# Optimization experiments

Hardware: AMD Instinct MI355X
Metric: run time of the kernel (lower is better)

The kernel has to match this reference:

```python
import jax, jax.numpy as jnp
import numpy as np

WINDOW = (2, 7, 7)
SHIFT = (1, 3, 3)
HEADS = 4


def _rel_pos_index(ws):
    coords = np.stack(np.meshgrid(*[np.arange(w) for w in ws], indexing='ij'))  # (3, wd, wh, ww)
    cf = coords.reshape(3, -1)
    rel = cf[:, :, None] - cf[:, None, :]  # (3, N, N)
    rel = rel.transpose(1, 2, 0).astype(np.int64)
    rel[:, :, 0] += ws[0] - 1
    rel[:, :, 1] += ws[1] - 1
    rel[:, :, 2] += ws[2] - 1
    rel[:, :, 0] *= (2 * ws[1] - 1) * (2 * ws[2] - 1)
    rel[:, :, 1] *= 2 * ws[2] - 1
    return rel.sum(-1)  # (N, N)


def _attn_mask(D, H, W, ws, ss):
    img = np.zeros((1, D, H, W, 1), np.float32)
    cnt = 0
    for d in (slice(None, -ws[0]), slice(-ws[0], -ss[0]), slice(-ss[0], None)):
        for h in (slice(None, -ws[1]), slice(-ws[1], -ss[1]), slice(-ss[1], None)):
            for w in (slice(None, -ws[2]), slice(-ws[2], -ss[2]), slice(-ss[2], None)):
                img[:, d, h, w, :] = cnt
                cnt += 1
    N = ws[0] * ws[1] * ws[2]
    mw = img.reshape(1, D // ws[0], ws[0], H // ws[1], ws[1], W // ws[2], ws[2], 1)
    mw = mw.transpose(0, 1, 3, 5, 2, 4, 6, 7).reshape(-1, N)  # (nW, N)
    diff = mw[:, None, :] - mw[:, :, None]
    return np.where(diff != 0, -100.0, 0.0).astype(np.float32)  # (nW, N, N)


def _win_partition(x, ws):
    B, D, H, W, C = x.shape
    x = x.reshape(B, D // ws[0], ws[0], H // ws[1], ws[1], W // ws[2], ws[2], C)
    return x.transpose(0, 1, 3, 5, 2, 4, 6, 7).reshape(-1, ws[0] * ws[1] * ws[2], C)


def _win_reverse(win, ws, B, D, H, W):
    C = win.shape[-1]
    x = win.reshape(B, D // ws[0], H // ws[1], W // ws[2], ws[0], ws[1], ws[2], C)
    return x.transpose(0, 1, 4, 2, 5, 3, 6, 7).reshape(B, D, H, W, C)


def _ln(x, w, b):
    mu = x.mean(-1, keepdims=True)
    var = x.var(-1, keepdims=True)
    return (x - mu) / jnp.sqrt(var + 1e-5) * w + b


def setup_inputs() -> dict:
    key = jax.random.key(0)
    ks = jax.random.split(key, 8)
    B, D, H, W, C = 4, 8, 56, 56, 128
    hidden = 4 * C
    table = (2 * WINDOW[0] - 1) * (2 * WINDOW[1] - 1) * (2 * WINDOW[2] - 1)
    return {
        'x': jax.random.normal(ks[0], (B, D, H, W, C), jnp.float32),
        'norm1_w': jnp.ones((C,), jnp.float32),
        'norm1_b': jnp.zeros((C,), jnp.float32),
        'qkv_w': 0.02 * jax.random.normal(ks[1], (3 * C, C), jnp.float32),
        'qkv_b': jnp.zeros((3 * C,), jnp.float32),
        'rpb': 0.02 * jax.random.normal(ks[2], (table, HEADS), jnp.float32),
        'proj_w': 0.02 * jax.random.normal(ks[3], (C, C), jnp.float32),
        'proj_b': jnp.zeros((C,), jnp.float32),
        'norm2_w': jnp.ones((C,), jnp.float32),
        'norm2_b': jnp.zeros((C,), jnp.float32),
        'fc1_w': 0.02 * jax.random.normal(ks[4], (hidden, C), jnp.float32),
        'fc1_b': jnp.zeros((hidden,), jnp.float32),
        'fc2_w': 0.02 * jax.random.normal(ks[5], (C, hidden), jnp.float32),
        'fc2_b': jnp.zeros((C,), jnp.float32),
    }


def reference(x, norm1_w, norm1_b, qkv_w, qkv_b, rpb, proj_w, proj_b,
              norm2_w, norm2_b, fc1_w, fc1_b, fc2_w, fc2_b):
    B, D, H, W, C = x.shape
    hd = C // HEADS
    scale = hd ** -0.5
    N = WINDOW[0] * WINDOW[1] * WINDOW[2]

    shortcut = x
    y = _ln(x, norm1_w, norm1_b)
    # cyclic shift (SW-MSA)
    y = jnp.roll(y, (-SHIFT[0], -SHIFT[1], -SHIFT[2]), axis=(1, 2, 3))
    win = _win_partition(y, WINDOW)  # (B_, N, C)
    B_ = win.shape[0]

    qkv = win @ qkv_w.T + qkv_b  # (B_, N, 3C)
    qkv = qkv.reshape(B_, N, 3, HEADS, hd).transpose(2, 0, 3, 1, 4)
    q, k, v = qkv[0] * scale, qkv[1], qkv[2]  # (B_, h, N, hd)

    attn = jnp.einsum('bhnd,bhmd->bhnm', q, k)  # (B_, h, N, N)
    rpi = _rel_pos_index(WINDOW)
    bias = rpb[rpi.reshape(-1)].reshape(N, N, HEADS).transpose(2, 0, 1)  # (h, N, N)
    attn = attn + bias[None]

    mask = jnp.asarray(_attn_mask(D, H, W, WINDOW, SHIFT))  # (nW, N, N)
    nW = mask.shape[0]
    attn = attn.reshape(B_ // nW, nW, HEADS, N, N) + mask[None, :, None]
    attn = jax.nn.softmax(attn.reshape(B_, HEADS, N, N), axis=-1)

    out = jnp.einsum('bhnm,bhmd->bhnd', attn, v)
    out = out.transpose(0, 2, 1, 3).reshape(B_, N, C)
    out = out @ proj_w.T + proj_b

    y = _win_reverse(out, WINDOW, B, D, H, W)
    y = jnp.roll(y, SHIFT, axis=(1, 2, 3))  # reverse cyclic shift
    x = shortcut + y

    h = _ln(x, norm2_w, norm2_b)
    h = jax.nn.gelu(h @ fc1_w.T + fc1_b, approximate=False)
    h = h @ fc2_w.T + fc2_b
    return x + h
```

## Files before the change

### kernel.cpp

```cpp
#include <hip/hip_runtime.h>
#include <math.h>

typedef short bf16x8 __attribute__((ext_vector_type(8)));
typedef float f32x4 __attribute__((ext_vector_type(4)));
typedef unsigned short u16;

#define DEVFN static __device__ __forceinline__

DEVFN u16 f2bf(float f) {
  union { float f; unsigned u; } v; v.f = f;
  return (u16)((v.u + 0x7FFFu + ((v.u >> 16) & 1u)) >> 16);
}

DEVFN void gload16(const void* g, void* l) {
  __builtin_amdgcn_global_load_lds(
      (const __attribute__((address_space(1))) void*)g,
      (__attribute__((address_space(3))) void*)l, 16, 0, 0);
}

DEVFN float gelu_tanh(float x) {
  float x2 = x * x;
  float m = x * fmaf(0.044715f, x2, 1.0f);
  float e = __expf(-1.5957691216057308f * m);
  return x / (1.0f + e);
}

#define TT 100352
#define BWIN 1024

__global__ void convert4_kernel(const float* __restrict__ a, const float* __restrict__ b,
                                const float* __restrict__ c, const float* __restrict__ d,
                                u16* __restrict__ oa, u16* __restrict__ ob,
                                u16* __restrict__ oc, u16* __restrict__ od) {
  int i = blockIdx.x * 256 + threadIdx.x;
  const float* s; u16* o; int off;
  if (i < 49152)       { s = a; o = oa; off = i; }
  else if (i < 65536)  { s = b; o = ob; off = i - 49152; }
  else if (i < 131072) { s = c; o = oc; off = i - 65536; }
  else                 { s = d; o = od; off = i - 131072; }
  o[off] = f2bf(s[off]);
}

__global__ void bias_kernel(const float* __restrict__ rpb, float* __restrict__ bias_full) {
  int idx = blockIdx.x * 256 + threadIdx.x;
  if (idx >= 4 * 9604) return;
  int h = idx / 9604, rem = idx % 9604, i = rem / 98, j = rem % 98;
  int di = i / 49, ri = i % 49, hi = ri / 7, wi = ri % 7;
  int dj = j / 49, rj = j % 49, hj = rj / 7, wj = rj % 7;
  int tidx = (di - dj + 1) * 169 + (hi - hj + 6) * 13 + (wi - wj + 6);
  bias_full[idx] = rpb[tidx * 4 + h];
}

template<int SHIFTED>
__global__ __launch_bounds__(256) void ln_kernel(const float* __restrict__ x,
    const float* __restrict__ w, const float* __restrict__ bterm, u16* __restrict__ out)
{
  int gw = blockIdx.x * 4 + (threadIdx.x >> 6);
  int lane = threadIdx.x & 63;
  size_t src;
  if (SHIFTED) {
    int b_ = gw / 98, n = gw % 98;
    int bb = b_ >> 8, widx = b_ & 255;
    int dw = widx >> 6, hw = (widx >> 3) & 7, ww = widx & 7;
    int dd = n / 49, rr = n % 49, hh = rr / 7, wn = rr % 7;
    int d = (dw * 2 + dd + 1) & 7;
    int h = hw * 7 + hh + 3; if (h >= 56) h -= 56;
    int wq = ww * 7 + wn + 3; if (wq >= 56) wq -= 56;
    src = ((size_t)(((bb * 8 + d) * 56 + h) * 56 + wq)) * 128;
  } else {
    src = (size_t)gw * 128;
  }
  float2 v = *(const float2*)(x + src + lane * 2);
  float s = v.x + v.y, q = v.x * v.x + v.y * v.y;
  #pragma unroll
  for (int m = 1; m < 64; m <<= 1) { s += __shfl_xor(s, m, 64); q += __shfl_xor(q, m, 64); }
  float mu = s * (1.0f / 128.0f);
  float var = q * (1.0f / 128.0f) - mu * mu;
  float rstd = rsqrtf(var + 1e-5f);
  int c = lane * 2;
  float y0 = (v.x - mu) * rstd * w[c] + bterm[c];
  float y1 = (v.y - mu) * rstd * w[c + 1] + bterm[c + 1];
  ushort2 o; o.x = f2bf(y0); o.y = f2bf(y1);
  *(ushort2*)(out + (size_t)gw * 128 + c) = o;
}

template<int EPI>
__global__ __launch_bounds__(256) void gemm_kernel(
    const u16* __restrict__ A, const u16* __restrict__ Bw,
    const float* __restrict__ bias, const float* __restrict__ res,
    void* __restrict__ outp, int M, int N, int K)
{
  __shared__ u16 smem[16384];
  u16* As = smem;
  u16* Bs = smem + 8192;
  const int m0 = blockIdx.x * 128, n0 = blockIdx.y * 128;
  const int t = threadIdx.x;
  const int wid = t >> 6, lane = t & 63;
  const int wr = wid >> 1, wc = wid & 1;
  const int l15 = lane & 15, lhi = lane >> 4;
  const int srow = lane >> 3;
  const int sslot = lane & 7;
  const int gcol = ((sslot ^ srow) << 3);
  f32x4 acc[4][4] = {};
  for (int k0 = 0; k0 < K; k0 += 64) {
    #pragma unroll
    for (int it = 0; it < 4; ++it) {
      const int rbase = it * 32 + wid * 8;
      const int row = rbase + srow;
      gload16(A + (size_t)(m0 + row) * K + k0 + gcol, As + rbase * 64);
      gload16(Bw + (size_t)(n0 + row) * K + k0 + gcol, Bs + rbase * 64);
    }
    __syncthreads();
    #pragma unroll
    for (int kk = 0; kk < 64; kk += 32) {
      bf16x8 af[4], bfr[4];
      const int csw = (kk + lhi * 8) ^ ((l15 & 7) << 3);
      #pragma unroll
      for (int mi = 0; mi < 4; ++mi) af[mi] = *(const bf16x8*)(As + (wr * 64 + mi * 16 + l15) * 64 + csw);
      #pragma unroll
      for (int ni = 0; ni < 4; ++ni) bfr[ni] = *(const bf16x8*)(Bs + (wc * 64 + ni * 16 + l15) * 64 + csw);
      #pragma unroll
      for (int mi = 0; mi < 4; ++mi)
        #pragma unroll
        for (int ni = 0; ni < 4; ++ni)
          acc[mi][ni] = __builtin_amdgcn_mfma_f32_16x16x32_bf16(af[mi], bfr[ni], acc[mi][ni], 0, 0, 0);
    }
    __syncthreads();
  }
  if (EPI == 0) {
    const float smul = (n0 == 0) ? 0.17677669529663689f : 1.0f;
    #pragma unroll
    for (int mi = 0; mi < 4; ++mi)
      #pragma unroll
      for (int ni = 0; ni < 4; ++ni) {
        int col = wc * 64 + ni * 16 + l15;
        float bcol = bias[n0 + col];
        #pragma unroll
        for (int r = 0; r < 4; ++r) {
          int row = wr * 64 + mi * 16 + lhi * 4 + r;
          float v = (acc[mi][ni][r] + bcol) * smul;
          smem[row * 128 + (((col >> 3) ^ (row & 7)) << 3) + (col & 7)] = f2bf(v);
        }
      }
    __syncthreads();
    const int rsub = t >> 4, sl = t & 15;
    #pragma unroll
    for (int j = 0; j < 8; ++j) {
      int row = j * 16 + rsub;
      int4 val = *(const int4*)(smem + row * 128 + ((sl ^ (row & 7)) << 3));
      *(int4*)((u16*)outp + (size_t)(m0 + row) * N + n0 + sl * 8) = val;
    }
  } else {
    #pragma unroll
    for (int mi = 0; mi < 4; ++mi)
      #pragma unroll
      for (int r = 0; r < 4; ++r) {
        int row = m0 + wr * 64 + mi * 16 + lhi * 4 + r;
        int b_ = row / 98, n = row % 98;
        int bb = b_ >> 8, widx = b_ & 255;
        int dw = widx >> 6, hw = (widx >> 3) & 7, ww = widx & 7;
        int dd = n / 49, rr = n % 49, hh = rr / 7, wn = rr % 7;
        int d = (dw * 2 + dd + 1) & 7;
        int h = hw * 7 + hh + 3; if (h >= 56) h -= 56;
        int wq = ww * 7 + wn + 3; if (wq >= 56) wq -= 56;
        size_t dbase = ((size_t)(((bb * 8 + d) * 56 + h) * 56 + wq)) * 128;
        #pragma unroll
        for (int ni = 0; ni < 4; ++ni) {
          int col = n0 + wc * 64 + ni * 16 + l15;
          float v = acc[mi][ni][r] + bias[col];
          ((float*)outp)[dbase + col] = res[dbase + col] + v;
        }
      }
  }
}

__global__ __launch_bounds__(256) void mlp_kernel(
    const u16* __restrict__ A, const u16* __restrict__ W1, const float* __restrict__ b1,
    const u16* __restrict__ W2, const float* __restrict__ b2,
    const float* __restrict__ res, float* __restrict__ outp)
{
  __shared__ u16 smem[32768];
  u16* As = smem;
  u16* Ws = smem + 8192;
  u16* Hs = smem + 24576;
  const int m0 = blockIdx.x * 64;
  const int t = threadIdx.x, wid = t >> 6, lane = t & 63;
  const int wr = wid >> 1, wc = wid & 1;
  const int l15 = lane & 15, lhi = lane >> 4;
  const int lrow4 = lane >> 4;
  const int lslot = lane & 15;

  #pragma unroll
  for (int i = 0; i < 4; ++i) {
    int row = i * 16 + wid * 4 + lrow4;
    gload16(A + (size_t)(m0 + row) * 128 + ((lslot ^ (row & 7)) << 3), As + i * 2048 + wid * 512);
  }
  #pragma unroll
  for (int i = 0; i < 8; ++i) {
    int row = i * 16 + wid * 4 + lrow4;
    gload16(W1 + (size_t)row * 128 + ((lslot ^ (row & 7)) << 3), Ws + i * 2048 + wid * 512);
  }
  f32x4 accO[2][4] = {};
  for (int hc = 0; hc < 4; ++hc) {
    __syncthreads();
    f32x4 accH[2][4] = {};
    #pragma unroll
    for (int kk = 0; kk < 128; kk += 32) {
      bf16x8 af[2], bfr[4];
      #pragma unroll
      for (int mi = 0; mi < 2; ++mi) {
        int row = wr * 32 + mi * 16 + l15;
        af[mi] = *(const bf16x8*)(As + row * 128 + (((((kk >> 3) + lhi)) ^ (row & 7)) << 3));
      }
      #pragma unroll
      for (int ni = 0; ni < 4; ++ni) {
        int row = wc * 64 + ni * 16 + l15;
        bfr[ni] = *(const bf16x8*)(Ws + row * 128 + (((((kk >> 3) + lhi)) ^ (row & 7)) << 3));
      }
      #pragma unroll
      for (int mi = 0; mi < 2; ++mi)
        #pragma unroll
        for (int ni = 0; ni < 4; ++ni)
          accH[mi][ni] = __builtin_amdgcn_mfma_f32_16x16x32_bf16(af[mi], bfr[ni], accH[mi][ni], 0, 0, 0);
    }
    __syncthreads();
    #pragma unroll
    for (int i = 0; i < 8; ++i) {
      int row = i * 16 + wid * 4 + lrow4;
      gload16(W2 + (size_t)row * 512 + hc * 128 + ((lslot ^ (row & 7)) << 3), Ws + i * 2048 + wid * 512);
    }
    #pragma unroll
    for (int mi = 0; mi < 2; ++mi)
      #pragma unroll
      for (int ni = 0; ni < 4; ++ni) {
        int hid = wc * 64 + ni * 16 + l15;
        float bb = b1[hc * 128 + hid];
        #pragma unroll
        for (int r = 0; r < 4; ++r) {
          int tok = wr * 32 + mi * 16 + lhi * 4 + r;
          float g = gelu_tanh(accH[mi][ni][r] + bb);
          Hs[tok * 128 + (((hid >> 3) ^ (tok & 7)) << 3) + (hid & 7)] = f2bf(g);
        }
      }
    __syncthreads();
    #pragma unroll
    for (int kk = 0; kk < 128; kk += 32) {
      bf16x8 af[2], bfr[4];
      #pragma unroll
      for (int mi = 0; mi < 2; ++mi) {
        int row = wr * 32 + mi * 16 + l15;
        af[mi] = *(const bf16x8*)(Hs + row * 128 + (((((kk >> 3) + lhi)) ^ (row & 7)) << 3));
      }
      #pragma unroll
      for (int ni = 0; ni < 4; ++ni) {
        int row = wc * 64 + ni * 16 + l15;
        bfr[ni] = *(const bf16x8*)(Ws + row * 128 + (((((kk >> 3) + lhi)) ^ (row & 7)) << 3));
      }
      #pragma unroll
      for (int mi = 0; mi < 2; ++mi)
        #pragma unroll
        for (int ni = 0; ni < 4; ++ni)
          accO[mi][ni] = __builtin_amdgcn_mfma_f32_16x16x32_bf16(af[mi], bfr[ni], accO[mi][ni], 0, 0, 0);
    }
    if (hc < 3) {
      __syncthreads();
      #pragma unroll
      for (int i = 0; i < 8; ++i) {
        int row = i * 16 + wid * 4 + lrow4;
        gload16(W1 + (size_t)((hc + 1) * 128 + row) * 128 + ((lslot ^ (row & 7)) << 3),
                Ws + i * 2048 + wid * 512);
      }
    }
  }
  #pragma unroll
  for (int mi = 0; mi < 2; ++mi)
    #pragma unroll
    for (int r = 0; r < 4; ++r) {
      int tok = m0 + wr * 32 + mi * 16 + lhi * 4 + r;
      #pragma unroll
      for (int ni = 0; ni < 4; ++ni) {
        int col = wc * 64 + ni * 16 + l15;
        size_t dst = (size_t)tok * 128 + col;
        outp[dst] = accO[mi][ni][r] + b2[col] + res[dst];
      }
    }
}

__global__ __launch_bounds__(64) void attn_kernel(
    const u16* __restrict__ qkv, const float* __restrict__ bias_full,
    u16* __restrict__ out_win)
{
  __shared__ u16 vT[32][136];
  __shared__ u16 P[16][136];
  __shared__ signed char rids[112];
  const int bid = blockIdx.x;
  const int w = bid >> 2, h = bid & 3;
  const int lane = threadIdx.x;
  const int l15 = lane & 15, lhi = lane >> 4;
  const int widx = w & 255;
  const int dw = widx >> 6, hw = (widx >> 3) & 7, ww = widx & 7;

  #pragma unroll
  for (int rep = 0; rep < 2; ++rep) {
    int t2 = lane + rep * 64;
    if (t2 < 112) {
      int rv = 0;
      if (t2 < 98) {
        int dd = t2 / 49, rr = t2 % 49, hh = rr / 7, wn = rr % 7;
        int dp = dw * 2 + dd, hp = hw * 7 + hh, wp = ww * 7 + wn;
        int rd = dp < 6 ? 0 : (dp < 7 ? 1 : 2);
        int rh = hp < 49 ? 0 : (hp < 53 ? 1 : 2);
        int rw2 = wp < 49 ? 0 : (wp < 53 ? 1 : 2);
        rv = rd * 9 + rh * 3 + rw2;
      }
      rids[t2] = (signed char)rv;
    }
  }
  for (int f = lane; f < 160; f += 64) {
    int d = f / 5, c = 96 + (f % 5) * 8;
    *(int4*)&vT[d][c] = (int4){0, 0, 0, 0};
  }
  if (lane < 48) {
    int r = lane / 3, c = 112 + (lane % 3) * 8;
    *(int4*)&P[r][c] = (int4){0, 0, 0, 0};
  }
  const size_t base = (size_t)w * 98 * 384;
  for (int f = lane; f < 392; f += 64) {
    int n = f >> 2, c = (f & 3) * 8;
    int4 v = *(const int4*)(qkv + base + (size_t)n * 384 + 256 + h * 32 + c);
    const u16* pv = (const u16*)&v;
    #pragma unroll
    for (int j = 0; j < 8; ++j) vT[c + j][n] = pv[j];
  }
  __syncthreads();

  const float* bh = bias_full + h * 9604;
  const size_t obase = (size_t)w * 98 * 128;
  for (int mt = 0; mt < 7; ++mt) {
    int qn = mt * 16 + l15; if (qn > 97) qn = 97;
    bf16x8 aq = *(const bf16x8*)(qkv + base + (size_t)qn * 384 + h * 32 + lhi * 8);
    f32x4 sf[7];
    #pragma unroll
    for (int nt = 0; nt < 7; ++nt) {
      int kn = nt * 16 + l15; if (kn > 97) kn = 97;
      bf16x8 bk = *(const bf16x8*)(qkv + base + (size_t)kn * 384 + 128 + h * 32 + lhi * 8);
      f32x4 z = {0.f, 0.f, 0.f, 0.f};
      sf[nt] = __builtin_amdgcn_mfma_f32_16x16x32_bf16(aq, bk, z, 0, 0, 0);
    }
    int irow[4], ridr[4];
    #pragma unroll
    for (int r = 0; r < 4; ++r) {
      irow[r] = mt * 16 + lhi * 4 + r;
      ridr[r] = rids[irow[r] > 111 ? 111 : irow[r]];
    }
    float mx[4] = {-1e30f, -1e30f, -1e30f, -1e30f};
    #pragma unroll
    for (int nt = 0; nt < 7; ++nt) {
      int j = nt * 16 + l15;
      int jc = j > 97 ? 97 : j;
      int rj = rids[j];
      #pragma unroll
      for (int r = 0; r < 4; ++r) {
        float s = sf[nt][r];
        int ic = irow[r] > 97 ? 97 : irow[r];
        s += bh[ic * 98 + jc];
        if (ridr[r] != rj) s -= 100.0f;
        if (j > 97) s = -1e30f;
        sf[nt][r] = s;
        mx[r] = fmaxf(mx[r], s);
      }
    }
    #pragma unroll
    for (int m = 1; m < 16; m <<= 1)
      #pragma unroll
      for (int r = 0; r < 4; ++r) mx[r] = fmaxf(mx[r], __shfl_xor(mx[r], m, 64));
    float sm[4] = {0.f, 0.f, 0.f, 0.f};
    #pragma unroll
    for (int nt = 0; nt < 7; ++nt)
      #pragma unroll
      for (int r = 0; r < 4; ++r) {
        float p = __expf(sf[nt][r] - mx[r]);
        sf[nt][r] = p;
        sm[r] += p;
      }
    #pragma unroll
    for (int m = 1; m < 16; m <<= 1)
      #pragma unroll
      for (int r = 0; r < 4; ++r) sm[r] += __shfl_xor(sm[r], m, 64);
    float inv[4];
    #pragma unroll
    for (int r = 0; r < 4; ++r) inv[r] = 1.0f / sm[r];
    __syncthreads();
    #pragma unroll
    for (int nt = 0; nt < 7; ++nt)
      #pragma unroll
      for (int r = 0; r < 4; ++r)
        P[lhi * 4 + r][nt * 16 + l15] = f2bf(sf[nt][r] * inv[r]);
    __syncthreads();
    f32x4 o0 = {}, o1 = {};
    #pragma unroll
    for (int ks = 0; ks < 4; ++ks) {
      bf16x8 ap  = *(const bf16x8*)(&P[l15][ks * 32 + lhi * 8]);
      bf16x8 bv0 = *(const bf16x8*)(&vT[l15][ks * 32 + lhi * 8]);
      bf16x8 bv1 = *(const bf16x8*)(&vT[16 + l15][ks * 32 + lhi * 8]);
      o0 = __builtin_amdgcn_mfma_f32_16x16x32_bf16(ap, bv0, o0, 0, 0, 0);
      o1 = __builtin_amdgcn_mfma_f32_16x16x32_bf16(ap, bv1, o1, 0, 0, 0);
    }
    #pragma unroll
    for (int r = 0; r < 4; ++r) {
      if (irow[r] < 98) {
        size_t orow = obase + (size_t)irow[r] * 128 + h * 32;
        out_win[orow + l15] = f2bf(o0[r]);
        out_win[orow + 16 + l15] = f2bf(o1[r]);
      }
    }
  }
}

extern "C" void kernel_launch(void* const* d_in, const int* in_sizes, int n_in,
                              void* d_out, int out_size, void* d_ws, size_t ws_size,
                              hipStream_t stream)
{
  const float* x      = (const float*)d_in[0];
  const float* n1w    = (const float*)d_in[1];
  const float* n1b    = (const float*)d_in[2];
  const float* qkv_w  = (const float*)d_in[3];
  const float* qkv_b  = (const float*)d_in[4];
  const float* rpb    = (const float*)d_in[5];
  const float* proj_w = (const float*)d_in[6];
  const float* proj_b = (const float*)d_in[7];
  const float* n2w    = (const float*)d_in[8];
  const float* n2b    = (const float*)d_in[9];
  const float* fc1_w  = (const float*)d_in[10];
  const float* fc1_b  = (const float*)d_in[11];
  const float* fc2_w  = (const float*)d_in[12];
  const float* fc2_b  = (const float*)d_in[13];

  char* p = (char*)d_ws;
  size_t off = 0;
  auto alloc = [&](size_t bytes) { void* r = p + off; off = (off + bytes + 255) & ~(size_t)255; return r; };
  u16*   qkvw_b    = (u16*)alloc(49152 * 2);
  u16*   projw_b   = (u16*)alloc(16384 * 2);
  u16*   fc1w_b    = (u16*)alloc(65536 * 2);
  u16*   fc2w_b    = (u16*)alloc(65536 * 2);
  float* bias_full = (float*)alloc(4 * 9604 * 4);
  u16*   y_win     = (u16*)alloc((size_t)TT * 128 * 2);
  float* x2        = (float*)alloc((size_t)TT * 128 * 4);
  u16*   h1        = (u16*)alloc((size_t)TT * 128 * 2);
  u16*   big       = (u16*)alloc((size_t)TT * 384 * 2);
  if (off > ws_size) return;

  convert4_kernel<<<768, 256, 0, stream>>>(qkv_w, proj_w, fc1_w, fc2_w,
                                           qkvw_b, projw_b, fc1w_b, fc2w_b);
  bias_kernel<<<(4 * 9604 + 255) / 256, 256, 0, stream>>>(rpb, bias_full);
  ln_kernel<1><<<TT / 4, 256, 0, stream>>>(x, n1w, n1b, y_win);
  gemm_kernel<0><<<dim3(TT / 128, 3), 256, 0, stream>>>(y_win, qkvw_b, qkv_b, nullptr, big, TT, 384, 128);
  attn_kernel<<<BWIN * 4, 64, 0, stream>>>(big, bias_full, y_win);
  gemm_kernel<1><<<dim3(TT / 128, 1), 256, 0, stream>>>(y_win, projw_b, proj_b, x, x2, TT, 128, 128);
  ln_kernel<0><<<TT / 4, 256, 0, stream>>>(x2, n2w, n2b, h1);
  mlp_kernel<<<TT / 64, 256, 0, stream>>>(h1, fc1w_b, fc1_b, fc2w_b, fc2_b, x2, (float*)d_out);
}
```

Baseline: 235.0 us.

## Restructure MLP kernel with 64-wide hidden chunks, register A, smaller LDS

The fused MLP kernel now processes the 512-wide hidden dimension in eight 64-wide chunks instead of four 128-wide chunks. It keeps the activation tile in registers rather than LDS and uses separate W1 and W2 chunk buffers, with W2 prefetched during the first GEMM. LDS drops from 64KB to 40KB and launch bounds request 4 blocks per CU, aiming for higher occupancy and better latency hiding. The cost is more barriers and chunk loads per block, and extra register pressure from holding A in registers.

```diff
diff --git a/kernel.cpp b/kernel.cpp
--- a/kernel.cpp
+++ b/kernel.cpp
@@ -174,101 +174,105 @@
   }
 }
 
-__global__ __launch_bounds__(256) void mlp_kernel(
+__global__ __launch_bounds__(256, 4) void mlp_kernel(
     const u16* __restrict__ A, const u16* __restrict__ W1, const float* __restrict__ b1,
     const u16* __restrict__ W2, const float* __restrict__ b2,
     const float* __restrict__ res, float* __restrict__ outp)
 {
-  __shared__ u16 smem[32768];
-  u16* As = smem;
-  u16* Ws = smem + 8192;
-  u16* Hs = smem + 24576;
+  __shared__ u16 smem[20480];
+  u16* W1c = smem;
+  u16* W2c = smem + 8192;
+  u16* Hs  = smem + 16384;
   const int m0 = blockIdx.x * 64;
   const int t = threadIdx.x, wid = t >> 6, lane = t & 63;
   const int wr = wid >> 1, wc = wid & 1;
   const int l15 = lane & 15, lhi = lane >> 4;
-  const int lrow4 = lane >> 4;
-  const int lslot = lane & 15;
+  const int srow4 = lane >> 4, sslot16 = lane & 15;
+  const int srow8 = lane >> 3, sslot8 = lane & 7;
 
   #pragma unroll
-  for (int i = 0; i < 4; ++i) {
-    int row = i * 16 + wid * 4 + lrow4;
-    gload16(A + (size_t)(m0 + row) * 128 + ((lslot ^ (row & 7)) << 3), As + i * 2048 + wid * 512);
-  }
+  for (int it = 0; it < 4; ++it) {
+    int rb1 = it * 16 + wid * 4;
+    gload16(W1 + (size_t)(rb1 + srow4) * 128 + ((sslot16 ^ ((rb1 + srow4) & 7)) << 3),
+            W1c + rb1 * 128);
+    int rb2 = it * 32 + wid * 8;
+    gload16(W2 + (size_t)(rb2 + srow8) * 512 + ((sslot8 ^ ((rb2 + srow8) & 7)) << 3),
+            W2c + rb2 * 64);
+  }
+  bf16x8 areg[2][4];
   #pragma unroll
-  for (int i = 0; i < 8; ++i) {
-    int row = i * 16 + wid * 4 + lrow4;
-    gload16(W1 + (size_t)row * 128 + ((lslot ^ (row & 7)) << 3), Ws + i * 2048 + wid * 512);
-  }
+  for (int mi = 0; mi < 2; ++mi)
+    #pragma unroll
+    for (int kg = 0; kg < 4; ++kg)
+      areg[mi][kg] = *(const bf16x8*)(A + (size_t)(m0 + wr * 32 + mi * 16 + l15) * 128 + kg * 32 + lhi * 8);
+
   f32x4 accO[2][4] = {};
-  for (int hc = 0; hc < 4; ++hc) {
-    __syncthreads();
-    f32x4 accH[2][4] = {};
-    #pragma unroll
-    for (int kk = 0; kk < 128; kk += 32) {
-      bf16x8 af[2], bfr[4];
-      #pragma unroll
-      for (int mi = 0; mi < 2; ++mi) {
-        int row = wr * 32 + mi * 16 + l15;
-        af[mi] = *(const bf16x8*)(As + row * 128 + (((((kk >> 3) + lhi)) ^ (row & 7)) << 3));
-      }
-      #pragma unroll
-      for (int ni = 0; ni < 4; ++ni) {
-        int row = wc * 64 + ni * 16 + l15;
-        bfr[ni] = *(const bf16x8*)(Ws + row * 128 + (((((kk >> 3) + lhi)) ^ (row & 7)) << 3));
+  __syncthreads();
+  for (int hc = 0; hc < 8; ++hc) {
+    f32x4 accH[2][2] = {};
+    #pragma unroll
+    for (int kk = 0; kk < 4; ++kk) {
+      bf16x8 bfr[2];
+      #pragma unroll
+      for (int ni = 0; ni < 2; ++ni) {
+        int row = wc * 32 + ni * 16 + l15;
+        bfr[ni] = *(const bf16x8*)(W1c + row * 128 + ((((kk * 4 + lhi) ^ (row & 7))) << 3));
       }
       #pragma unroll
       for (int mi = 0; mi < 2; ++mi)
         #pragma unroll
-        for (int ni = 0; ni < 4; ++ni)
-          accH[mi][ni] = __builtin_amdgcn_mfma_f32_16x16x32_bf16(af[mi], bfr[ni], accH[mi][ni], 0, 0, 0);
-    }
-    __syncthreads();
-    #pragma unroll
-    for (int i = 0; i < 8; ++i) {
-      int row = i * 16 + wid * 4 + lrow4;
-      gload16(W2 + (size_t)row * 512 + hc * 128 + ((lslot ^ (row & 7)) << 3), Ws + i * 2048 + wid * 512);
+        for (int ni = 0; ni < 2; ++ni)
+          accH[mi][ni] = __builtin_amdgcn_mfma_f32_16x16x32_bf16(areg[mi][kk], bfr[ni], accH[mi][ni], 0, 0, 0);
+    }
+    __syncthreads();
+    if (hc < 7) {
+      #pragma unroll
+      for (int it = 0; it < 4; ++it) {
+        int rb1 = it * 16 + wid * 4;
+        gload16(W1 + (size_t)((hc + 1) * 64 + rb1 + srow4) * 128 + ((sslot16 ^ ((rb1 + srow4) & 7)) << 3),
+                W1c + rb1 * 128);
+      }
     }
     #pragma unroll
     for (int mi = 0; mi < 2; ++mi)
       #pragma unroll
-      for (int ni = 0; ni < 4; ++ni) {
-        int hid = wc * 64 + ni * 16 + l15;
-        float bb = b1[hc * 128 + hid];
+      for (int ni = 0; ni < 2; ++ni) {
+        int hid = wc * 32 + ni * 16 + l15;
+        float bb = b1[hc * 64 + hid];
         #pragma unroll
         for (int r = 0; r < 4; ++r) {
           int tok = wr * 32 + mi * 16 + lhi * 4 + r;
           float g = gelu_tanh(accH[mi][ni][r] + bb);
-          Hs[tok * 128 + (((hid >> 3) ^ (tok & 7)) << 3) + (hid & 7)] = f2bf(g);
+          Hs[tok * 64 + ((((hid >> 3) ^ (tok & 7))) << 3) + (hid & 7)] = f2bf(g);
         }
       }
     __syncthreads();
     #pragma unroll
-    for (int kk = 0; kk < 128; kk += 32) {
-      bf16x8 af[2], bfr[4];
+    for (int kk = 0; kk < 2; ++kk) {
+      bf16x8 ah[2], bfr[4];
       #pragma unroll
       for (int mi = 0; mi < 2; ++mi) {
         int row = wr * 32 + mi * 16 + l15;
-        af[mi] = *(const bf16x8*)(Hs + row * 128 + (((((kk >> 3) + lhi)) ^ (row & 7)) << 3));
+        ah[mi] = *(const bf16x8*)(Hs + row * 64 + ((((kk * 4 + lhi) ^ (row & 7))) << 3));
       }
       #pragma unroll
       for (int ni = 0; ni < 4; ++ni) {
         int row = wc * 64 + ni * 16 + l15;
-        bfr[ni] = *(const bf16x8*)(Ws + row * 128 + (((((kk >> 3) + lhi)) ^ (row & 7)) << 3));
+        bfr[ni] = *(const bf16x8*)(W2c + row * 64 + ((((kk * 4 + lhi) ^ (row & 7))) << 3));
       }
       #pragma unroll
       for (int mi = 0; mi < 2; ++mi)
         #pragma unroll
         for (int ni = 0; ni < 4; ++ni)
-          accO[mi][ni] = __builtin_amdgcn_mfma_f32_16x16x32_bf16(af[mi], bfr[ni], accO[mi][ni], 0, 0, 0);
-    }
-    if (hc < 3) {
-      __syncthreads();
-      #pragma unroll
-      for (int i = 0; i < 8; ++i) {
-        int row = i * 16 + wid * 4 + lrow4;
-        gload16(W1 + (size_t)((hc + 1) * 128 + row) * 128 + ((lslot ^ (row & 7)) << 3),
-                Ws + i * 2048 + wid * 512);
+          accO[mi][ni] = __builtin_amdgcn_mfma_f32_16x16x32_bf16(ah[mi], bfr[ni], accO[mi][ni], 0, 0, 0);
+    }
+    __syncthreads();
+    if (hc < 7) {
+      #pragma unroll
+      for (int it = 0; it < 4; ++it) {
+        int rb2 = it * 32 + wid * 8;
+        gload16(W2 + (size_t)(rb2 + srow8) * 512 + (hc + 1) * 64 + ((sslot8 ^ ((rb2 + srow8) & 7)) << 3),
+                W2c + rb2 * 64);
       }
     }
   }
```

Result: slower. 251.5 us (+7.0%).
